# Performance work log

Hardware: AMD Instinct MI355X
Metric: run time of the kernel (lower is better)

## Reference

```python
import jax, jax.numpy as jnp
import numpy as np

DIMS = 1024
HEAD = 16
HEAD_DIM = DIMS // HEAD
B, S = 1, 2048


def setup_inputs() -> dict:
    key = jax.random.key(0)
    ks = jax.random.split(key, 8)
    init = lambda k, shape: (jax.random.normal(k, shape, dtype=jnp.float32) * 0.02)
    x = jax.random.normal(ks[0], (B, S, DIMS), dtype=jnp.float32)
    mask = jnp.zeros((S, S), dtype=jnp.float32)
    Wq = init(ks[1], (DIMS, DIMS)); bq = jnp.zeros((DIMS,), jnp.float32)
    Wk = init(ks[2], (DIMS, DIMS))  # k projection has no bias
    Wv = init(ks[3], (DIMS, DIMS)); bv = jnp.zeros((DIMS,), jnp.float32)
    Wo = init(ks[4], (DIMS, DIMS)); bo = jnp.zeros((DIMS,), jnp.float32)
    Zfactor = jnp.asarray(1e-05, dtype=jnp.float32)
    inv_freq = 1.0 / (10000.0 ** (jnp.arange(0, HEAD_DIM, 2, dtype=jnp.float32) / HEAD_DIM))
    return {"x": x, "mask": mask, "Wq": Wq, "bq": bq, "Wk": Wk, "Wv": Wv,
            "bv": bv, "Wo": Wo, "bo": bo, "Zfactor": Zfactor, "inv_freq": inv_freq}


def _apply_rotary(u, cos, sin):
    # u: [B,H,S,hd]; cos/sin: [S,hd/2]. Pairs are consecutive (view_as_complex).
    a = u[..., 0::2]
    b = u[..., 1::2]
    ra = a * cos - b * sin
    rb = a * sin + b * cos
    return jnp.stack([ra, rb], axis=-1).reshape(u.shape)


def reference(x, mask, Wq, bq, Wk, Wv, bv, Wo, bo, Zfactor, inv_freq):
    Bx, Sx, D = x.shape
    H, hd = HEAD, D // HEAD
    q = x @ Wq.T + bq
    k = x @ Wk.T          # no bias on k
    v = x @ Wv.T + bv
    # [B,S,D] -> [B,H,S,hd]
    split = lambda u: u.reshape(Bx, Sx, H, hd).transpose(0, 2, 1, 3)
    q, k, v = split(q), split(k), split(v)
    # RoPE frequencies: t outer inv_freq -> [S, hd/2]
    t = jnp.arange(Sx, dtype=jnp.float32)
    freqs = t[:, None] * inv_freq[None, :]
    cos, sin = jnp.cos(freqs), jnp.sin(freqs)
    q = _apply_rotary(q, cos, sin)
    k = _apply_rotary(k, cos, sin)
    scale = hd ** (-0.25)
    qk = jnp.einsum('bhqd,bhkd->bhqk', q * scale, k * scale)
    # custom zscale: pad positions (token id 0 taken as first feature of k) get tiny factor
    token_ids = k[..., 0]  # [B,H,Sk]
    zfactor = jnp.clip(jax.nn.softplus(Zfactor), 1e-05, 0.0001)
    zscale = jnp.where(token_ids == 0.0, zfactor, 1.0)  # [B,H,Sk]
    qk = qk + mask[None, None, :Sx, :Sx] * zscale[:, :, None, :]
    qk = qk * zscale[:, :, None, :]
    w = jax.nn.softmax(qk, axis=-1)
    wv = jnp.einsum('bhqk,bhkd->bhqd', w, v)
    wv = wv.transpose(0, 2, 1, 3).reshape(Bx, Sx, D)
    out = wv @ Wo.T + bo
    return out, qk
```

## Files before the change

### kernel.cpp

```cpp
#include <hip/hip_runtime.h>
#include <hip/hip_bf16.h>

#define SEQ 2048
#define DIM 1024
#define NH  16
#define HD  64
#define SPLIT 4
#define KCOLS (SEQ / SPLIT)
#define KVBLK 128
#define CREF 10.0f

typedef __bf16 bf16_t;
typedef __bf16 bf16x4 __attribute__((ext_vector_type(4)));
typedef __bf16 bf16x8 __attribute__((ext_vector_type(8)));
typedef float  f32x4  __attribute__((ext_vector_type(4)));

#define MFMA16(a,b,c) __builtin_amdgcn_mfma_f32_16x16x32_bf16((a),(b),(c),0,0,0)

__device__ __forceinline__ void gload_lds16(const void* g, void* l) {
    __builtin_amdgcn_global_load_lds(
        (const __attribute__((address_space(1))) unsigned int*)g,
        (__attribute__((address_space(3))) unsigned int*)l, 16, 0, 0);
}

__global__ __launch_bounds__(256) void k_tables(const float* __restrict__ invf,
                                                float* __restrict__ cosT,
                                                float* __restrict__ sinT,
                                                int* __restrict__ flag) {
    int id = blockIdx.x * 256 + threadIdx.x;
    if (id == 0) flag[0] = 0;
    int t = id >> 5, i = id & 31;
    float f = (float)t * invf[i];
    cosT[id] = cosf(f);
    sinT[id] = sinf(f);
}

__global__ __launch_bounds__(256) void k_maskchk(const float* __restrict__ mask,
                                                 int* __restrict__ flag) {
    int id = blockIdx.x * 256 + threadIdx.x;
    f32x4 v = *(const f32x4*)(mask + (size_t)id * 4);
    bool nz = (v[0] != 0.f) | (v[1] != 0.f) | (v[2] != 0.f) | (v[3] != 0.f);
    if (__any(nz) && (threadIdx.x & 63) == 0) atomicOr(flag, 1);
}

__global__ __launch_bounds__(256) void k_cvt_all(const float* __restrict__ x,
                                                 const float* __restrict__ Wq,
                                                 const float* __restrict__ Wk,
                                                 const float* __restrict__ Wv,
                                                 const float* __restrict__ Wo,
                                                 bf16_t* __restrict__ Xb,
                                                 bf16_t* __restrict__ Wqkvb,
                                                 bf16_t* __restrict__ Wob) {
    int id = blockIdx.x * 256 + threadIdx.x;
    const float* src;
    bf16_t* dst;
    int off;
    if (id < 524288)       { src = x;  dst = Xb;              off = id; }
    else if (id < 786432)  { src = Wq; dst = Wqkvb;           off = id - 524288; }
    else if (id < 1048576) { src = Wk; dst = Wqkvb + 1048576; off = id - 786432; }
    else if (id < 1310720) { src = Wv; dst = Wqkvb + 2097152; off = id - 1048576; }
    else                   { src = Wo; dst = Wob;             off = id - 1310720; }
    float4 v = ((const float4*)src)[off];
    bf16x4 o;
    o[0] = (bf16_t)v.x; o[1] = (bf16_t)v.y; o[2] = (bf16_t)v.z; o[3] = (bf16_t)v.w;
    ((bf16x4*)dst)[off] = o;
}

__global__ __launch_bounds__(256) void k_biasqkv(const float* __restrict__ bq,
                                                 const float* __restrict__ bv,
                                                 float* __restrict__ bqkv) {
    int n = blockIdx.x * 256 + threadIdx.x;
    bqkv[n] = (n < 1024) ? bq[n] : ((n < 2048) ? 0.0f : bv[n - 2048]);
}

__global__ __launch_bounds__(256) void gemm128(const bf16_t* __restrict__ A,
                                               const bf16_t* __restrict__ W,
                                               const float* __restrict__ bias,
                                               bf16_t* __restrict__ outBf,
                                               float* __restrict__ outF,
                                               int N, int K) {
    __shared__ __align__(16) bf16_t As[2][128 * 32];
    __shared__ __align__(16) bf16_t Bs[2][128 * 32];
    int tid = threadIdx.x, wid = tid >> 6, lane = tid & 63;
    int lrow = lane >> 4, lcol = lane & 15;
    int wr = wid >> 1, wc = wid & 1;

    int orig = blockIdx.y * gridDim.x + blockIdx.x;
    int cpx = (gridDim.x * gridDim.y) >> 3;
    int swzb = (orig & 7) * cpx + (orig >> 3);
    int m0 = (swzb % gridDim.x) * 128;
    int n0 = (swzb / gridDim.x) * 128;

    int sr = wid * 32 + (lane >> 2);
    int sc = (lane & 3) * 8;
    const bf16_t* Ag = A + (size_t)(m0 + sr) * K + sc;
    const bf16_t* Wg = W + (size_t)(n0 + sr) * K + sc;

    f32x4 acc[4][4] = {};

#define STAGE(buf, k0) do { \
        gload_lds16(Ag + (k0),          &As[buf][wid * 1024]);       \
        gload_lds16(Ag + 16 * K + (k0), &As[buf][wid * 1024 + 512]); \
        gload_lds16(Wg + (k0),          &Bs[buf][wid * 1024]);       \
        gload_lds16(Wg + 16 * K + (k0), &Bs[buf][wid * 1024 + 512]); \
    } while (0)

    STAGE(0, 0);
    __syncthreads();
    int buf = 0;
    for (int k0 = 0; k0 < K; k0 += 32) {
        if (k0 + 32 < K) STAGE(buf ^ 1, k0 + 32);
        bf16x8 af[4], bfr[4];
#pragma unroll
        for (int mi = 0; mi < 4; mi++)
            af[mi] = *(const bf16x8*)&As[buf][(wr * 64 + mi * 16 + lcol) * 32 + lrow * 8];
#pragma unroll
        for (int ni = 0; ni < 4; ni++)
            bfr[ni] = *(const bf16x8*)&Bs[buf][(wc * 64 + ni * 16 + lcol) * 32 + lrow * 8];
#pragma unroll
        for (int mi = 0; mi < 4; mi++)
#pragma unroll
            for (int ni = 0; ni < 4; ni++)
                acc[mi][ni] = MFMA16(af[mi], bfr[ni], acc[mi][ni]);
        __syncthreads();
        buf ^= 1;
    }
#undef STAGE
#pragma unroll
    for (int ni = 0; ni < 4; ni++) {
        int col = n0 + wc * 64 + ni * 16 + lcol;
        float bb = bias ? bias[col] : 0.0f;
#pragma unroll
        for (int mi = 0; mi < 4; mi++)
#pragma unroll
            for (int j = 0; j < 4; j++) {
                int row = m0 + wr * 64 + mi * 16 + lrow * 4 + j;
                float v = acc[mi][ni][j] + bb;
                if (outBf) outBf[(size_t)row * N + col] = (bf16_t)v;
                else       outF [(size_t)row * N + col] = v;
            }
    }
}

__global__ __launch_bounds__(256) void k_rope(const bf16_t* __restrict__ QKV,
                                              const float* __restrict__ cosT,
                                              const float* __restrict__ sinT,
                                              const float* __restrict__ Zf,
                                              bf16_t* __restrict__ Qh,
                                              bf16_t* __restrict__ Kh,
                                              float* __restrict__ zsq) {
    int id = blockIdx.x * 256 + threadIdx.x;
    int s = id >> 9, pp = id & 511;
    int h = pp >> 5, i = pp & 31;
    float c  = cosT[s * 32 + i];
    float sn = sinT[s * 32 + i];
    const float scale = 0.3535533905932738f;
    size_t qb = (size_t)s * 3072 + h * HD + 2 * i;
    size_t kb = qb + 1024;
    size_t ob = ((size_t)h * SEQ + s) * HD + 2 * i;

    float qa = (float)QKV[qb], qbv = (float)QKV[qb + 1];
    Qh[ob]     = (bf16_t)((qa * c - qbv * sn) * scale);
    Qh[ob + 1] = (bf16_t)((qa * sn + qbv * c) * scale);

    float k0a = (float)QKV[(size_t)s * 3072 + 1024 + h * HD];
    float k0b = (float)QKV[(size_t)s * 3072 + 1024 + h * HD + 1];
    float ra0 = k0a * cosT[s * 32] - k0b * sinT[s * 32];
    float z = Zf[0];
    float zfac = fminf(fmaxf(log1pf(__expf(z)), 1e-5f), 1e-4f);
    float zs = (ra0 == 0.0f) ? zfac : 1.0f;

    float ka = (float)QKV[kb], kbv = (float)QKV[kb + 1];
    float ra = ka * c - kbv * sn;
    float rb = ka * sn + kbv * c;
    Kh[ob]     = (bf16_t)(ra * scale * zs);
    Kh[ob + 1] = (bf16_t)(rb * scale * zs);
    if (i == 0) zsq[h * SEQ + s] = zs * zs;
}

__global__ __launch_bounds__(256) void k_transpose(const bf16_t* __restrict__ QKV,
                                                   bf16_t* __restrict__ Vt) {
    __shared__ bf16_t tile[64][66];
    int t = threadIdx.x;
    int c = t & 63, r4 = t >> 6;
    int s0 = blockIdx.x * 64, d0 = blockIdx.y * 64;
#pragma unroll
    for (int i = 0; i < 16; i++) {
        int r = i * 4 + r4;
        tile[r][c] = QKV[(size_t)(s0 + r) * 3072 + 2048 + d0 + c];
    }
    __syncthreads();
#pragma unroll
    for (int i = 0; i < 16; i++) {
        int r = i * 4 + r4;
        Vt[(size_t)(d0 + r) * SEQ + s0 + c] = tile[c][r];
    }
}

__global__ __launch_bounds__(256) void k_attn(const bf16_t* __restrict__ Qh,
                                              const bf16_t* __restrict__ Kh,
                                              const bf16_t* __restrict__ Vt,
                                              const float* __restrict__ mask,
                                              const float* __restrict__ zsq,
                                              const int* __restrict__ mflag,
                                              float* __restrict__ qk_out,
                                              bf16_t* __restrict__ Opart,
                                              float* __restrict__ Lpart) {
    __shared__ __align__(16) char Ks[16384];
    __shared__ __align__(16) char Vs[16384];
    __shared__ __align__(16) char Plds[4][4096];
    int tid = threadIdx.x, wid = tid >> 6, lane = tid & 63;
    int lrow = lane >> 4, lcol = lane & 15;

    int orig = blockIdx.x;
    int s = (orig & 7) * 256 + (orig >> 3);
    int h = s >> 7;
    int rem = s & 127;
    int qblk = rem & 31, sp = rem >> 5;

    int q0 = qblk * 64 + wid * 16;
    int kbase = sp * KCOLS;
    int mz = mflag[0];

    bf16x8 aq[2];
    {
        const bf16_t* qb = Qh + ((size_t)h * SEQ + q0 + lcol) * HD + lrow * 8;
        aq[0] = *(const bf16x8*)qb;
        aq[1] = *(const bf16x8*)(qb + 32);
    }

    float l = 0.f;
    f32x4 acc[4] = {};
    char* wl = &Plds[wid][0];
    float* qkbase = qk_out + (size_t)h * SEQ * SEQ;
    const float* mrow = mask + (size_t)(q0 + lcol) * SEQ;
    const bf16_t* khead = Kh + (size_t)h * SEQ * HD;
    const bf16_t* vthead = Vt + (size_t)h * HD * SEQ;
    const float*  zrow  = zsq + h * SEQ;
    int swzP = (lcol & 7) << 4;
    int l7 = lcol & 7;

    int so[4], krk[4], ksk[4], vrv[4], vsv[4];
#pragma unroll
    for (int i = 0; i < 4; i++) {
        int o = wid * 4096 + i * 1024 + lane * 16;
        so[i] = wid * 4096 + i * 1024;
        krk[i] = o >> 7;
        ksk[i] = ((o >> 4) & 7) ^ (krk[i] & 7);
        vrv[i] = o >> 8;
        int cv = (o >> 4) & 15;
        vsv[i] = (cv & 8) | ((cv & 7) ^ (vrv[i] & 7));
    }

    for (int kc = kbase; kc < kbase + KCOLS; kc += KVBLK) {
#pragma unroll
        for (int i = 0; i < 4; i++) {
            gload_lds16(khead + (size_t)(kc + krk[i]) * HD + ksk[i] * 8, Ks + so[i]);
            gload_lds16(vthead + (size_t)vrv[i] * SEQ + kc + vsv[i] * 8,  Vs + so[i]);
        }
        __syncthreads();

        float p[8][4];
#pragma unroll
        for (int ct = 0; ct < 8; ct++) {
            int row = ct * 16 + lcol;
            int a0 = row * 128 + ((lrow ^ l7) << 4);
            bf16x8 k0 = *(const bf16x8*)(Ks + a0);
            bf16x8 k1 = *(const bf16x8*)(Ks + (a0 ^ 64));
            f32x4 cacc = {};
            cacc = MFMA16(k0, aq[0], cacc);
            cacc = MFMA16(k1, aq[1], cacc);
#pragma unroll
            for (int j = 0; j < 4; j++) p[ct][j] = cacc[j];
        }
        if (mz) {
#pragma unroll
            for (int ct = 0; ct < 8; ct++) {
                int k4 = kc + ct * 16 + lrow * 4;
                f32x4 mv = *(const f32x4*)(mrow + k4);
                f32x4 zv = *(const f32x4*)(zrow + k4);
#pragma unroll
                for (int j = 0; j < 4; j++)
                    p[ct][j] = fmaf(mv[j], zv[j], p[ct][j]);
            }
        }
#pragma unroll
        for (int ct = 0; ct < 8; ct++) {
            bf16x4 pk;
#pragma unroll
            for (int j = 0; j < 4; j++) {
                float e = __expf(p[ct][j] - CREF);
                l += e;
                pk[j] = (bf16_t)e;
            }
            int addr = (lcol << 8) + ((ct * 16 + lrow * 4) << 1);
            *(bf16x4*)(wl + (addr ^ swzP)) = pk;
        }
        bf16x8 pa[4];
#pragma unroll
        for (int ks = 0; ks < 4; ks++) {
            int addr = (lcol << 8) + (ks << 6) + (lrow << 4);
            pa[ks] = *(const bf16x8*)(wl + (addr ^ swzP));
        }
        __builtin_amdgcn_s_setprio(1);
#pragma unroll
        for (int ks = 0; ks < 4; ks++) {
            int c = ks * 4 + lrow;
            int cs = (c & 8) | ((c & 7) ^ l7);
#pragma unroll
            for (int ng = 0; ng < 4; ng++) {
                int a = (ng * 16 + lcol) * 256 + (cs << 4);
                bf16x8 bv = *(const bf16x8*)(Vs + a);
                acc[ng] = MFMA16(bv, pa[ks], acc[ng]);
            }
        }
        __builtin_amdgcn_s_setprio(0);
#pragma unroll
        for (int ct = 0; ct < 8; ct++) {
            int k4 = kc + ct * 16 + lrow * 4;
            f32x4 ov;
#pragma unroll
            for (int j = 0; j < 4; j++) ov[j] = p[ct][j];
            *(f32x4*)(qkbase + (size_t)(q0 + lcol) * SEQ + k4) = ov;
        }
        __syncthreads();
    }
#pragma unroll
    for (int ng = 0; ng < 4; ng++) {
        bf16x4 o4;
#pragma unroll
        for (int j = 0; j < 4; j++) o4[j] = (bf16_t)acc[ng][j];
        size_t idx = ((size_t)(h * SEQ + q0 + lcol) * SPLIT + sp) * HD + ng * 16 + lrow * 4;
        *(bf16x4*)(Opart + idx) = o4;
    }
    l += __shfl_xor(l, 16);
    l += __shfl_xor(l, 32);
    if (lane < 16) {
        Lpart[((size_t)h * SEQ + q0 + lane) * SPLIT + sp] = l;
    }
}

__global__ __launch_bounds__(256) void k_combine(const bf16_t* __restrict__ Opart,
                                                 const float* __restrict__ Lpart,
                                                 bf16_t* __restrict__ wv) {
    int gid = blockIdx.x * 256 + threadIdx.x;
    int rowIdx = gid >> 6, d = gid & 63;
    const float* lp = Lpart + (size_t)rowIdx * SPLIT;
    float L = 0.f, O = 0.f;
    const bf16_t* ob = Opart + (size_t)rowIdx * SPLIT * HD + d;
#pragma unroll
    for (int s = 0; s < SPLIT; s++) {
        L += lp[s];
        O += (float)ob[(size_t)s * HD];
    }
    int h = rowIdx >> 11, row = rowIdx & (SEQ - 1);
    wv[(size_t)row * DIM + h * HD + d] = (bf16_t)(O / L);
}

extern "C" void kernel_launch(void* const* d_in, const int* in_sizes, int n_in,
                              void* d_out, int out_size, void* d_ws, size_t ws_size,
                              hipStream_t stream) {
    const float* x    = (const float*)d_in[0];
    const float* mask = (const float*)d_in[1];
    const float* Wq   = (const float*)d_in[2];
    const float* bq   = (const float*)d_in[3];
    const float* Wk   = (const float*)d_in[4];
    const float* Wv   = (const float*)d_in[5];
    const float* bv   = (const float*)d_in[6];
    const float* Wo   = (const float*)d_in[7];
    const float* bo   = (const float*)d_in[8];
    const float* Zf   = (const float*)d_in[9];
    const float* invf = (const float*)d_in[10];

    char* ws = (char*)d_ws;
    size_t off = 0;
    auto alloc = [&](size_t bytes) -> char* {
        char* p = ws + off;
        off += (bytes + 255) & ~(size_t)255;
        return p;
    };
    float*  cosT  = (float*)alloc(65536 * 4);
    float*  sinT  = (float*)alloc(65536 * 4);
    bf16_t* Xb    = (bf16_t*)alloc((size_t)SEQ * DIM * 2);
    bf16_t* Wqkvb = (bf16_t*)alloc((size_t)3 * DIM * DIM * 2);
    bf16_t* Wob   = (bf16_t*)alloc((size_t)DIM * DIM * 2);
    float*  bqkv  = (float*)alloc(3072 * 4);
    bf16_t* QKV   = (bf16_t*)alloc((size_t)SEQ * 3 * DIM * 2);
    bf16_t* Qhp   = (bf16_t*)alloc((size_t)SEQ * DIM * 2);
    bf16_t* Khp   = (bf16_t*)alloc((size_t)SEQ * DIM * 2);
    bf16_t* Vt    = (bf16_t*)alloc((size_t)DIM * SEQ * 2);
    float*  zsq   = (float*)alloc((size_t)NH * SEQ * 4);
    bf16_t* Opart = (bf16_t*)alloc((size_t)NH * SEQ * SPLIT * HD * 2);
    float*  Lpart = (float*)alloc((size_t)NH * SEQ * SPLIT * 4);
    bf16_t* WVb   = (bf16_t*)alloc((size_t)SEQ * DIM * 2);
    int*    mflag = (int*)alloc(256);

    float* outp = (float*)d_out;
    float* qkp  = outp + (size_t)SEQ * DIM;

    k_tables<<<256, 256, 0, stream>>>(invf, cosT, sinT, mflag);
    k_maskchk<<<(SEQ * SEQ / 4) / 256, 256, 0, stream>>>(mask, mflag);
    k_cvt_all<<<6144, 256, 0, stream>>>(x, Wq, Wk, Wv, Wo, Xb, Wqkvb, Wob);
    k_biasqkv<<<12, 256, 0, stream>>>(bq, bv, bqkv);

    gemm128<<<dim3(SEQ / 128, 3072 / 128), 256, 0, stream>>>(Xb, Wqkvb, bqkv, QKV, nullptr, 3072, DIM);

    k_rope<<<(SEQ * 512) / 256, 256, 0, stream>>>(QKV, cosT, sinT, Zf, Qhp, Khp, zsq);
    k_transpose<<<dim3(SEQ / 64, NH), 256, 0, stream>>>(QKV, Vt);

    k_attn<<<NH * (SEQ / 64) * SPLIT, 256, 0, stream>>>(Qhp, Khp, Vt, mask, zsq, mflag,
                                                        qkp, Opart, Lpart);
    k_combine<<<(NH * SEQ * HD) / 256, 256, 0, stream>>>(Opart, Lpart, WVb);

    gemm128<<<dim3(SEQ / 128, DIM / 128), 256, 0, stream>>>(WVb, Wob, bo, nullptr, outp, DIM, DIM);
}
```

Baseline: 154.4 us.

## Merge small prep kernels and reuse K tile LDS for softmax staging

```diff
diff --git a/kernel.cpp b/kernel.cpp
--- a/kernel.cpp
+++ b/kernel.cpp
@@ -24,23 +24,20 @@
 }
 
 __global__ __launch_bounds__(256) void k_tables(const float* __restrict__ invf,
+                                                const float* __restrict__ bq,
+                                                const float* __restrict__ bv,
                                                 float* __restrict__ cosT,
                                                 float* __restrict__ sinT,
+                                                float* __restrict__ bqkv,
                                                 int* __restrict__ flag) {
     int id = blockIdx.x * 256 + threadIdx.x;
     if (id == 0) flag[0] = 0;
+    if (id < 3072)
+        bqkv[id] = (id < 1024) ? bq[id] : ((id < 2048) ? 0.0f : bv[id - 2048]);
     int t = id >> 5, i = id & 31;
     float f = (float)t * invf[i];
     cosT[id] = cosf(f);
     sinT[id] = sinf(f);
-}
-
-__global__ __launch_bounds__(256) void k_maskchk(const float* __restrict__ mask,
-                                                 int* __restrict__ flag) {
-    int id = blockIdx.x * 256 + threadIdx.x;
-    f32x4 v = *(const f32x4*)(mask + (size_t)id * 4);
-    bool nz = (v[0] != 0.f) | (v[1] != 0.f) | (v[2] != 0.f) | (v[3] != 0.f);
-    if (__any(nz) && (threadIdx.x & 63) == 0) atomicOr(flag, 1);
 }
 
 __global__ __launch_bounds__(256) void k_cvt_all(const float* __restrict__ x,
@@ -48,10 +45,20 @@
                                                  const float* __restrict__ Wk,
                                                  const float* __restrict__ Wv,
                                                  const float* __restrict__ Wo,
+                                                 const float* __restrict__ mask,
                                                  bf16_t* __restrict__ Xb,
                                                  bf16_t* __restrict__ Wqkvb,
-                                                 bf16_t* __restrict__ Wob) {
-    int id = blockIdx.x * 256 + threadIdx.x;
+                                                 bf16_t* __restrict__ Wob,
+                                                 int* __restrict__ flag) {
+    int bid = blockIdx.x;
+    if (bid >= 6144) {
+        int id = (bid - 6144) * 256 + threadIdx.x;
+        f32x4 v = *(const f32x4*)(mask + (size_t)id * 4);
+        bool nz = (v[0] != 0.f) | (v[1] != 0.f) | (v[2] != 0.f) | (v[3] != 0.f);
+        if (__any(nz) && (threadIdx.x & 63) == 0) atomicOr(flag, 1);
+        return;
+    }
+    int id = bid * 256 + threadIdx.x;
     const float* src;
     bf16_t* dst;
     int off;
@@ -66,13 +73,6 @@
     ((bf16x4*)dst)[off] = o;
 }
 
-__global__ __launch_bounds__(256) void k_biasqkv(const float* __restrict__ bq,
-                                                 const float* __restrict__ bv,
-                                                 float* __restrict__ bqkv) {
-    int n = blockIdx.x * 256 + threadIdx.x;
-    bqkv[n] = (n < 1024) ? bq[n] : ((n < 2048) ? 0.0f : bv[n - 2048]);
-}
-
 __global__ __launch_bounds__(256) void gemm128(const bf16_t* __restrict__ A,
                                                const bf16_t* __restrict__ W,
                                                const float* __restrict__ bias,
@@ -142,14 +142,35 @@
     }
 }
 
-__global__ __launch_bounds__(256) void k_rope(const bf16_t* __restrict__ QKV,
-                                              const float* __restrict__ cosT,
-                                              const float* __restrict__ sinT,
-                                              const float* __restrict__ Zf,
-                                              bf16_t* __restrict__ Qh,
-                                              bf16_t* __restrict__ Kh,
-                                              float* __restrict__ zsq) {
-    int id = blockIdx.x * 256 + threadIdx.x;
+__global__ __launch_bounds__(256) void k_ropeT(const bf16_t* __restrict__ QKV,
+                                               const float* __restrict__ cosT,
+                                               const float* __restrict__ sinT,
+                                               const float* __restrict__ Zf,
+                                               bf16_t* __restrict__ Qh,
+                                               bf16_t* __restrict__ Kh,
+                                               float* __restrict__ zsq,
+                                               bf16_t* __restrict__ Vt) {
+    __shared__ bf16_t tile[64][66];
+    int bid = blockIdx.x;
+    if (bid >= 4096) {
+        int tb = bid - 4096;
+        int t = threadIdx.x;
+        int c = t & 63, r4 = t >> 6;
+        int s0 = (tb & 31) * 64, d0 = (tb >> 5) * 64;
+#pragma unroll
+        for (int i = 0; i < 16; i++) {
+            int r = i * 4 + r4;
+            tile[r][c] = QKV[(size_t)(s0 + r) * 3072 + 2048 + d0 + c];
+        }
+        __syncthreads();
+#pragma unroll
+        for (int i = 0; i < 16; i++) {
+            int r = i * 4 + r4;
+            Vt[(size_t)(d0 + r) * SEQ + s0 + c] = tile[c][r];
+        }
+        return;
+    }
+    int id = bid * 256 + threadIdx.x;
     int s = id >> 9, pp = id & 511;
     int h = pp >> 5, i = pp & 31;
     float c  = cosT[s * 32 + i];
@@ -176,25 +197,6 @@
     Kh[ob]     = (bf16_t)(ra * scale * zs);
     Kh[ob + 1] = (bf16_t)(rb * scale * zs);
     if (i == 0) zsq[h * SEQ + s] = zs * zs;
-}
-
-__global__ __launch_bounds__(256) void k_transpose(const bf16_t* __restrict__ QKV,
-                                                   bf16_t* __restrict__ Vt) {
-    __shared__ bf16_t tile[64][66];
-    int t = threadIdx.x;
-    int c = t & 63, r4 = t >> 6;
-    int s0 = blockIdx.x * 64, d0 = blockIdx.y * 64;
-#pragma unroll
-    for (int i = 0; i < 16; i++) {
-        int r = i * 4 + r4;
-        tile[r][c] = QKV[(size_t)(s0 + r) * 3072 + 2048 + d0 + c];
-    }
-    __syncthreads();
-#pragma unroll
-    for (int i = 0; i < 16; i++) {
-        int r = i * 4 + r4;
-        Vt[(size_t)(d0 + r) * SEQ + s0 + c] = tile[c][r];
-    }
 }
 
 __global__ __launch_bounds__(256) void k_attn(const bf16_t* __restrict__ Qh,
@@ -208,7 +210,6 @@
                                               float* __restrict__ Lpart) {
     __shared__ __align__(16) char Ks[16384];
     __shared__ __align__(16) char Vs[16384];
-    __shared__ __align__(16) char Plds[4][4096];
     int tid = threadIdx.x, wid = tid >> 6, lane = tid & 63;
     int lrow = lane >> 4, lcol = lane & 15;
 
@@ -231,7 +232,7 @@
 
     float l = 0.f;
     f32x4 acc[4] = {};
-    char* wl = &Plds[wid][0];
+    char* wl = Ks + wid * 4096;
     float* qkbase = qk_out + (size_t)h * SEQ * SEQ;
     const float* mrow = mask + (size_t)(q0 + lcol) * SEQ;
     const bf16_t* khead = Kh + (size_t)h * SEQ * HD;
@@ -284,6 +285,8 @@
                     p[ct][j] = fmaf(mv[j], zv[j], p[ct][j]);
             }
         }
+        __syncthreads();
+
 #pragma unroll
         for (int ct = 0; ct < 8; ct++) {
             bf16x4 pk;
@@ -398,15 +401,12 @@
     float* outp = (float*)d_out;
     float* qkp  = outp + (size_t)SEQ * DIM;
 
-    k_tables<<<256, 256, 0, stream>>>(invf, cosT, sinT, mflag);
-    k_maskchk<<<(SEQ * SEQ / 4) / 256, 256, 0, stream>>>(mask, mflag);
-    k_cvt_all<<<6144, 256, 0, stream>>>(x, Wq, Wk, Wv, Wo, Xb, Wqkvb, Wob);
-    k_biasqkv<<<12, 256, 0, stream>>>(bq, bv, bqkv);
+    k_tables<<<256, 256, 0, stream>>>(invf, bq, bv, cosT, sinT, bqkv, mflag);
+    k_cvt_all<<<10240, 256, 0, stream>>>(x, Wq, Wk, Wv, Wo, mask, Xb, Wqkvb, Wob, mflag);
 
     gemm128<<<dim3(SEQ / 128, 3072 / 128), 256, 0, stream>>>(Xb, Wqkvb, bqkv, QKV, nullptr, 3072, DIM);
 
-    k_rope<<<(SEQ * 512) / 256, 256, 0, stream>>>(QKV, cosT, sinT, Zf, Qhp, Khp, zsq);
-    k_transpose<<<dim3(SEQ / 64, NH), 256, 0, stream>>>(QKV, Vt);
+    k_ropeT<<<4608, 256, 0, stream>>>(QKV, cosT, sinT, Zf, Qhp, Khp, zsq, Vt);
 
     k_attn<<<NH * (SEQ / 64) * SPLIT, 256, 0, stream>>>(Qhp, Khp, Vt, mask, zsq, mflag,
                                                         qkp, Opart, Lpart);
```

New measurement: 151.2 us (median of 2 runs). 2.1% less time.
